# Performance work log

Measured on AMD Instinct MI355X. Metric: run time of the kernel, lower is better.

The kernel has to match this reference:

```python
import jax, jax.numpy as jnp
import numpy as np

B, D_IN, D_OUT, P = 4096, 1024, 1024, 16


def setup_inputs() -> dict:
    key = jax.random.key(0)
    k_x, k_A, k_b, k_W, k_c = jax.random.split(key, 5)
    return {
        "x": jax.random.normal(k_x, (B, D_IN), dtype=jnp.float32),
        "A": jax.random.normal(k_A, (P, D_IN, D_IN), dtype=jnp.float32),
        "b": jax.random.normal(k_b, (P, D_IN), dtype=jnp.float32),
        "W": jax.random.normal(k_W, (P, D_OUT, D_IN), dtype=jnp.float32),
        "c": jax.random.normal(k_c, (P, D_OUT), dtype=jnp.float32),
    }


def reference(x, A, b, W, c):
    # membership: sigmoid(-sum_k((A[p] x)_k - b[p,k])) == sigmoid(-(x . A[p].sum(rows) - b[p].sum()))
    scores = jnp.einsum("bd,pkd->bp", x, A) - jnp.sum(b, axis=1)  # (B, P)
    m = jax.nn.sigmoid(-scores)
    m = m / (jnp.sum(m, axis=1, keepdims=True) + 1e-6)            # (B, P)
    # combine: sum_p m[b,p] * (x @ W[p].T + c[p])
    out = jnp.einsum("bp,pod,bd->bo", m, W, x) + m @ c            # (B, D_OUT)
    return out
```

## Files before the change

### kernel.cpp

```cpp
#include <hip/hip_runtime.h>
#include <hip/hip_bf16.h>
#include <stdint.h>


typedef __attribute__((ext_vector_type(4))) float f32x4;
typedef __attribute__((ext_vector_type(8))) short bf16x8;

#define WBF_OFF   0u
#define XBF_OFF   33554432u
#define ASUM_OFF  41943040u
#define BSUM_OFF  42008576u
#define M_OFF     42008832u
#define APART_OFF 44040192u
#define PART_OFF  50331648u

__device__ __forceinline__ unsigned short f2bf(float f) {
  unsigned u = __builtin_bit_cast(unsigned, f);
  unsigned r = (u + 0x7fffu + ((u >> 16) & 1u)) >> 16;
  return (unsigned short)r;
}

__device__ __forceinline__ void gload_lds16(const void* g, void* l) {
  __builtin_amdgcn_global_load_lds(
      (const __attribute__((address_space(1))) void*)g,
      (__attribute__((address_space(3))) void*)l, 16, 0, 0);
}

__global__ void asum_part(const float* __restrict__ A, float* __restrict__ apart) {
  const int p = blockIdx.x >> 4, kc = blockIdx.x & 15;
  const int t = threadIdx.x;
  const float4* Ap = (const float4*)(A + (size_t)p * 1048576 + (size_t)kc * 65536);
  float sx = 0.f, sy = 0.f, sz = 0.f, sw = 0.f;
#pragma unroll 8
  for (int k = 0; k < 64; ++k) {
    float4 v = Ap[k * 256 + t];
    sx += v.x; sy += v.y; sz += v.z; sw += v.w;
  }
  ((float4*)apart)[((size_t)kc * 16 + p) * 256 + t] = make_float4(sx, sy, sz, sw);
}

__global__ void asum_final(const float* __restrict__ apart, const float* __restrict__ b,
                           float* __restrict__ Asum, float* __restrict__ bsum) {
  const int p = blockIdx.x;
  const int t = threadIdx.x;
  float4 acc = make_float4(0.f, 0.f, 0.f, 0.f);
#pragma unroll
  for (int kc = 0; kc < 16; ++kc) {
    float4 v = ((const float4*)apart)[((size_t)kc * 16 + p) * 256 + t];
    acc.x += v.x; acc.y += v.y; acc.z += v.z; acc.w += v.w;
  }
  ((float4*)(Asum + p * 1024))[t] = acc;
  float4 bv = ((const float4*)b)[(size_t)p * 256 + t];
  float s = bv.x + bv.y + bv.z + bv.w;
  __shared__ float red[256];
  red[t] = s;
  __syncthreads();
  for (int off = 128; off > 0; off >>= 1) {
    if (t < off) red[t] += red[t + off];
    __syncthreads();
  }
  if (t == 0) bsum[p] = red[0];
}

__global__ void convert_bf16(const float* __restrict__ src,
                             unsigned short* __restrict__ dst, int n4) {
  int i = blockIdx.x * blockDim.x + threadIdx.x;
  const int stride = gridDim.x * blockDim.x;
  for (; i < n4; i += stride) {
    float4 v = ((const float4*)src)[i];
    uint2 o;
    o.x = (unsigned)f2bf(v.x) | ((unsigned)f2bf(v.y) << 16);
    o.y = (unsigned)f2bf(v.z) | ((unsigned)f2bf(v.w) << 16);
    ((uint2*)dst)[i] = o;
  }
}

__global__ void memberships_fused(const float* __restrict__ x, const float* __restrict__ Asum,
                                  const float* __restrict__ bsum, float* __restrict__ m,
                                  unsigned short* __restrict__ xbf) {
  const int wave = threadIdx.x >> 6, lane = threadIdx.x & 63;
  const int b = blockIdx.x * 4 + wave;
  const float4* xrow4 = (const float4*)(x + (size_t)b * 1024);
  float4 xv[4];
#pragma unroll
  for (int i = 0; i < 4; ++i) xv[i] = xrow4[i * 64 + lane];
  ushort4* xbo = (ushort4*)(xbf + (size_t)b * 1024);
#pragma unroll
  for (int i = 0; i < 4; ++i) {
    ushort4 h;
    h.x = f2bf(xv[i].x); h.y = f2bf(xv[i].y);
    h.z = f2bf(xv[i].z); h.w = f2bf(xv[i].w);
    xbo[i * 64 + lane] = h;
  }
  float myE = 0.f, sumE = 0.f;
#pragma unroll
  for (int p = 0; p < 16; ++p) {
    const float4* ap4 = (const float4*)(Asum + p * 1024);
    float s = 0.f;
#pragma unroll
    for (int i = 0; i < 4; ++i) {
      float4 av = ap4[i * 64 + lane];
      s += xv[i].x * av.x + xv[i].y * av.y + xv[i].z * av.z + xv[i].w * av.w;
    }
#pragma unroll
    for (int off = 32; off > 0; off >>= 1) s += __shfl_xor(s, off, 64);
    const float score = s - bsum[p];
    const float e = 1.f / (1.f + __expf(score));
    sumE += e;
    if ((lane & 15) == p) myE = e;
  }
  const float mv = myE / (sumE + 1e-6f);
  if (lane < 16) m[(size_t)b * 16 + lane] = mv;
}

template <bool SPLIT>
__global__ __launch_bounds__(256, 2) void moe_gemm(
    const unsigned short* __restrict__ xbf,
    const unsigned short* __restrict__ wbf,
    const float* __restrict__ mptr,
    const float* __restrict__ c,
    float* __restrict__ dst)
{
  __shared__ __align__(16) unsigned char lds[2 * 16384];
  __shared__ __align__(16) float m_lds[128 * 16];

  const int tid = threadIdx.x;
  const int bid = blockIdx.x;
  const int s = SPLIT ? (bid >> 8) : 0;
  const int tile = bid & 255;
  const int bt = tile >> 3, ot = tile & 7;
  const int brow = bt << 7, ocol = ot << 7;
  const int p0 = s * 8;
  const int PC = SPLIT ? 8 : 16;

  const int lane = tid & 63;
  const int wv = tid >> 6;
  const int wr = wv >> 1, wc = wv & 1;

  {
    const float4* msrc = (const float4*)(mptr + (size_t)brow * 16);
    float4* mdst = (float4*)m_lds;
    mdst[tid] = msrc[tid];
    mdst[256 + tid] = msrc[256 + tid];
  }

  auto stage = [&](int buf, int u) {
    const int p = p0 + (u >> 5);
    const int k0 = (u & 31) << 5;
    const unsigned short* Ag = xbf + (size_t)brow * 1024 + k0;
    const unsigned short* Bg = wbf + (size_t)p * 1048576 + (size_t)ocol * 1024 + k0;
    unsigned char* base = lds + buf * 16384;
#pragma unroll
    for (int r = 0; r < 4; ++r) {
      const int e = ((r & 1) << 8) + tid;
      const int row = e >> 2, seg = e & 3;
      const unsigned short* g = (r < 2 ? Ag : Bg) + (size_t)row * 1024 + seg * 8;
      unsigned char* l = base + (r >= 2 ? 8192 : 0) +
                         ((((r & 1) << 8) + (tid & ~63)) << 4);
      gload_lds16(g, l);
    }
  };

  auto compute = [&](int buf, f32x4 (&acc)[4][4]) {
    const unsigned char* base = lds + buf * 16384;
    const unsigned char* Ab = base + ((wr * 64 + (lane & 15)) << 6) + ((lane >> 4) << 4);
    const unsigned char* Bb = base + 8192 + ((wc * 64 + (lane & 15)) << 6) + ((lane >> 4) << 4);
    bf16x8 a[4], b[4];
#pragma unroll
    for (int i = 0; i < 4; ++i) {
      a[i] = *(const bf16x8*)(Ab + i * 1024);
      b[i] = *(const bf16x8*)(Bb + i * 1024);
    }
#pragma unroll
    for (int mi = 0; mi < 4; ++mi)
#pragma unroll
      for (int ni = 0; ni < 4; ++ni)
        acc[mi][ni] = __builtin_amdgcn_mfma_f32_16x16x32_bf16(a[mi], b[ni], acc[mi][ni], 0, 0, 0);
  };

  const f32x4 zv = {0.f, 0.f, 0.f, 0.f};
  f32x4 master[4][4];
#pragma unroll
  for (int mi = 0; mi < 4; ++mi)
#pragma unroll
    for (int ni = 0; ni < 4; ++ni) master[mi][ni] = zv;

  int cur = 0;
  stage(0, 0);

  for (int pi = 0; pi < PC; ++pi) {
    const int p = p0 + pi;
    f32x4 acc[4][4];
#pragma unroll
    for (int mi = 0; mi < 4; ++mi)
#pragma unroll
      for (int ni = 0; ni < 4; ++ni) acc[mi][ni] = zv;

#pragma unroll 2
    for (int ks = 0; ks < 32; ++ks) {
      const int u = pi * 32 + ks;
      __syncthreads();
      if (u + 1 < PC * 32) stage(cur ^ 1, u + 1);
      compute(cur, acc);
      cur ^= 1;
    }

    float cvn[4] = {0.f, 0.f, 0.f, 0.f};
    if constexpr (!SPLIT) {
#pragma unroll
      for (int ni = 0; ni < 4; ++ni)
        cvn[ni] = c[(size_t)p * 1024 + ocol + wc * 64 + ni * 16 + (lane & 15)];
    }
#pragma unroll
    for (int mi = 0; mi < 4; ++mi)
#pragma unroll
      for (int j = 0; j < 4; ++j) {
        const int lrow = wr * 64 + mi * 16 + ((lane >> 4) << 2) + j;
        const float ms = m_lds[lrow * 16 + p];
#pragma unroll
        for (int ni = 0; ni < 4; ++ni) {
          if constexpr (SPLIT) master[mi][ni][j] += ms * acc[mi][ni][j];
          else                 master[mi][ni][j] += ms * (acc[mi][ni][j] + cvn[ni]);
        }
      }
  }

  float* ob = SPLIT ? (dst + (size_t)s * 4194304) : dst;
#pragma unroll
  for (int mi = 0; mi < 4; ++mi)
#pragma unroll
    for (int j = 0; j < 4; ++j) {
      const int grow = brow + wr * 64 + mi * 16 + ((lane >> 4) << 2) + j;
#pragma unroll
      for (int ni = 0; ni < 4; ++ni) {
        const int gcol = ocol + wc * 64 + ni * 16 + (lane & 15);
        ob[(size_t)grow * 1024 + gcol] = master[mi][ni][j];
      }
    }
}

__global__ void reduce_out(const float* __restrict__ part, const float* __restrict__ m,
                           const float* __restrict__ c, float* __restrict__ out) {
  const int b = blockIdx.x;
  const int t = threadIdx.x;
  __shared__ float msh[16];
  if (t < 16) msh[t] = m[(size_t)b * 16 + t];
  __syncthreads();
  const int o = t * 4;
  const float* p0 = part + (size_t)b * 1024;
  const float* p1 = part + 4194304 + (size_t)b * 1024;
  float4 a = *(const float4*)(p0 + o);
  float4 bq = *(const float4*)(p1 + o);
  float rx = a.x + bq.x, ry = a.y + bq.y, rz = a.z + bq.z, rw = a.w + bq.w;
#pragma unroll
  for (int p = 0; p < 16; ++p) {
    const float mp = msh[p];
    float4 cv = *(const float4*)(c + (size_t)p * 1024 + o);
    rx += mp * cv.x; ry += mp * cv.y; rz += mp * cv.z; rw += mp * cv.w;
  }
  *(float4*)(out + (size_t)b * 1024 + o) = make_float4(rx, ry, rz, rw);
}

extern "C" void kernel_launch(void* const* d_in, const int* in_sizes, int n_in,
                              void* d_out, int out_size, void* d_ws, size_t ws_size,
                              hipStream_t stream) {
  const float* x = (const float*)d_in[0];
  const float* A = (const float*)d_in[1];
  const float* b = (const float*)d_in[2];
  const float* W = (const float*)d_in[3];
  const float* c = (const float*)d_in[4];
  float* out = (float*)d_out;
  char* ws = (char*)d_ws;

  unsigned short* wbf = (unsigned short*)(ws + WBF_OFF);
  unsigned short* xbf = (unsigned short*)(ws + XBF_OFF);
  float* Asum = (float*)(ws + ASUM_OFF);
  float* bsum = (float*)(ws + BSUM_OFF);
  float* mm = (float*)(ws + M_OFF);
  float* apart = (float*)(ws + APART_OFF);
  float* part = (float*)(ws + PART_OFF);

  asum_part<<<256, 256, 0, stream>>>(A, apart);
  asum_final<<<16, 256, 0, stream>>>(apart, b, Asum, bsum);
  convert_bf16<<<4096, 256, 0, stream>>>(W, wbf, 16777216 / 4);
  memberships_fused<<<1024, 256, 0, stream>>>(x, Asum, bsum, mm, xbf);

  if (ws_size >= (size_t)PART_OFF + 2ull * 16777216ull) {
    moe_gemm<true><<<512, 256, 0, stream>>>(xbf, wbf, mm, c, part);
    reduce_out<<<4096, 256, 0, stream>>>(part, mm, c, out);
  } else {
    moe_gemm<false><<<256, 256, 0, stream>>>(xbf, wbf, mm, c, out);
  }
}
```

Baseline: 377.9 us.

## Split MoE GEMM across K halves into four partial slabs

Adds a 4-way split of the MoE GEMM (2 expert groups × 2 K halves), launching 1024 blocks instead of 512 and writing four fp32 partial slabs that reduce_out sums. The aim is more parallelism and better CU occupancy on a GPU with many CUs, where 512 blocks may leave CUs underused. The cost is twice the partial-output traffic to write and read back, and the new path only runs when the workspace is large enough.

```diff
diff --git a/kernel.cpp b/kernel.cpp
--- a/kernel.cpp
+++ b/kernel.cpp
@@ -113,7 +113,7 @@
   if (lane < 16) m[(size_t)b * 16 + lane] = mv;
 }
 
-template <bool SPLIT>
+template <int NSLAB>
 __global__ __launch_bounds__(256, 2) void moe_gemm(
     const unsigned short* __restrict__ xbf,
     const unsigned short* __restrict__ wbf,
@@ -126,12 +126,17 @@
 
   const int tid = threadIdx.x;
   const int bid = blockIdx.x;
-  const int s = SPLIT ? (bid >> 8) : 0;
   const int tile = bid & 255;
   const int bt = tile >> 3, ot = tile & 7;
   const int brow = bt << 7, ocol = ot << 7;
-  const int p0 = s * 8;
-  const int PC = SPLIT ? 8 : 16;
+
+  const int sg = (NSLAB == 4) ? ((bid >> 8) & 1) : (NSLAB == 2 ? (bid >> 8) : 0);
+  const int kh = (NSLAB == 4) ? (bid >> 9) : 0;
+  const int PC = (NSLAB >= 2) ? 8 : 16;
+  const int p0 = sg * 8;
+  const int KSTEPS = (NSLAB == 4) ? 16 : 32;
+  const int kbase = kh * 512;
+  const int TOT = PC * KSTEPS;
 
   const int lane = tid & 63;
   const int wv = tid >> 6;
@@ -145,8 +150,8 @@
   }
 
   auto stage = [&](int buf, int u) {
-    const int p = p0 + (u >> 5);
-    const int k0 = (u & 31) << 5;
+    const int p = p0 + (u / KSTEPS);
+    const int k0 = kbase + (u % KSTEPS) * 32;
     const unsigned short* Ag = xbf + (size_t)brow * 1024 + k0;
     const unsigned short* Bg = wbf + (size_t)p * 1048576 + (size_t)ocol * 1024 + k0;
     unsigned char* base = lds + buf * 16384;
@@ -197,16 +202,16 @@
       for (int ni = 0; ni < 4; ++ni) acc[mi][ni] = zv;
 
 #pragma unroll 2
-    for (int ks = 0; ks < 32; ++ks) {
-      const int u = pi * 32 + ks;
+    for (int ks = 0; ks < KSTEPS; ++ks) {
+      const int u = pi * KSTEPS + ks;
       __syncthreads();
-      if (u + 1 < PC * 32) stage(cur ^ 1, u + 1);
+      if (u + 1 < TOT) stage(cur ^ 1, u + 1);
       compute(cur, acc);
       cur ^= 1;
     }
 
     float cvn[4] = {0.f, 0.f, 0.f, 0.f};
-    if constexpr (!SPLIT) {
+    if constexpr (NSLAB == 1) {
 #pragma unroll
       for (int ni = 0; ni < 4; ++ni)
         cvn[ni] = c[(size_t)p * 1024 + ocol + wc * 64 + ni * 16 + (lane & 15)];
@@ -219,13 +224,14 @@
         const float ms = m_lds[lrow * 16 + p];
 #pragma unroll
         for (int ni = 0; ni < 4; ++ni) {
-          if constexpr (SPLIT) master[mi][ni][j] += ms * acc[mi][ni][j];
-          else                 master[mi][ni][j] += ms * (acc[mi][ni][j] + cvn[ni]);
+          if constexpr (NSLAB == 1) master[mi][ni][j] += ms * (acc[mi][ni][j] + cvn[ni]);
+          else                      master[mi][ni][j] += ms * acc[mi][ni][j];
         }
       }
   }
 
-  float* ob = SPLIT ? (dst + (size_t)s * 4194304) : dst;
+  const int slab = (NSLAB == 4) ? (kh * 2 + sg) : sg;
+  float* ob = dst + (size_t)slab * 4194304;
 #pragma unroll
   for (int mi = 0; mi < 4; ++mi)
 #pragma unroll
@@ -239,6 +245,7 @@
     }
 }
 
+template <int NSLAB>
 __global__ void reduce_out(const float* __restrict__ part, const float* __restrict__ m,
                            const float* __restrict__ c, float* __restrict__ out) {
   const int b = blockIdx.x;
@@ -247,11 +254,12 @@
   if (t < 16) msh[t] = m[(size_t)b * 16 + t];
   __syncthreads();
   const int o = t * 4;
-  const float* p0 = part + (size_t)b * 1024;
-  const float* p1 = part + 4194304 + (size_t)b * 1024;
-  float4 a = *(const float4*)(p0 + o);
-  float4 bq = *(const float4*)(p1 + o);
-  float rx = a.x + bq.x, ry = a.y + bq.y, rz = a.z + bq.z, rw = a.w + bq.w;
+  float rx = 0.f, ry = 0.f, rz = 0.f, rw = 0.f;
+#pragma unroll
+  for (int s = 0; s < NSLAB; ++s) {
+    float4 a = *(const float4*)(part + (size_t)s * 4194304 + (size_t)b * 1024 + o);
+    rx += a.x; ry += a.y; rz += a.z; rw += a.w;
+  }
 #pragma unroll
   for (int p = 0; p < 16; ++p) {
     const float mp = msh[p];
@@ -285,10 +293,15 @@
   convert_bf16<<<4096, 256, 0, stream>>>(W, wbf, 16777216 / 4);
   memberships_fused<<<1024, 256, 0, stream>>>(x, Asum, bsum, mm, xbf);
 
-  if (ws_size >= (size_t)PART_OFF + 2ull * 16777216ull) {
-    moe_gemm<true><<<512, 256, 0, stream>>>(xbf, wbf, mm, c, part);
-    reduce_out<<<4096, 256, 0, stream>>>(part, mm, c, out);
+  const size_t need4 = (size_t)PART_OFF + 4ull * 16777216ull;
+  const size_t need2 = (size_t)PART_OFF + 2ull * 16777216ull;
+  if (ws_size >= need4) {
+    moe_gemm<4><<<1024, 256, 0, stream>>>(xbf, wbf, mm, c, part);
+    reduce_out<4><<<4096, 256, 0, stream>>>(part, mm, c, out);
+  } else if (ws_size >= need2) {
+    moe_gemm<2><<<512, 256, 0, stream>>>(xbf, wbf, mm, c, part);
+    reduce_out<2><<<4096, 256, 0, stream>>>(part, mm, c, out);
   } else {
-    moe_gemm<false><<<256, 256, 0, stream>>>(xbf, wbf, mm, c, out);
-  }
-}
+    moe_gemm<1><<<256, 256, 0, stream>>>(xbf, wbf, mm, c, out);
+  }
+}
```

Result: faster. 368.4 us (-2.5%).
